# Performance work log

Hardware: AMD Instinct MI355X
Metric: run time of the kernel (lower is better)

## Reference

```python
import jax, jax.numpy as jnp
import numpy as np

IN_SZ = 256
OUT_SZ = 256
N_CHAN = 1024
RANK = 4  # min(4, IN_SZ*OUT_SZ)
B = 256
N = 2048


def setup_inputs() -> dict:
    key = jax.random.key(0)
    k_x, k_idx, k_u, k_v, k_b = jax.random.split(key, 5)
    x = jax.random.normal(k_x, (B, N, IN_SZ), dtype=jnp.float32)
    indices = jax.random.randint(k_idx, (B,), 0, N_CHAN)
    # init per reset_parameters(const=1.0)
    bound_u = np.sqrt(3.0 / RANK)              # fan_out of weights_U [C, r] is r
    weights_U = jax.random.uniform(k_u, (N_CHAN, RANK), jnp.float32, -bound_u, bound_u)
    bound_v = np.sqrt(1.0 / (IN_SZ * OUT_SZ))  # fan_out of weights_V [r, in*out]
    weights_V = jax.random.uniform(k_v, (RANK, IN_SZ * OUT_SZ), jnp.float32, -bound_v, bound_v)
    bound_b = np.sqrt(1.0 / RANK)
    bias = jax.random.uniform(k_b, (N_CHAN, 1, OUT_SZ), jnp.float32, -bound_b, bound_b)
    return {"x": x, "indices": indices, "weights_U": weights_U,
            "weights_V": weights_V, "bias": bias}


def reference(x, indices, weights_U, weights_V, bias):
    # weight synthesis: gather U rows first, then low-rank expand (same math as
    # full (U@V)[indices], without materializing unused channels)
    w = (weights_U[indices] @ weights_V).reshape(-1, IN_SZ, OUT_SZ)  # [B, in, out]
    out = jnp.einsum('bni,bio->bno', x, w)                            # [B, N, out]
    out = out + bias[indices]                                         # [B,1,out] broadcast
    return out
```

## Files before the change

kernel.cpp:

```cpp
#include <hip/hip_runtime.h>
#include <cstdint>

typedef __attribute__((ext_vector_type(8))) short short8;
typedef __attribute__((ext_vector_type(4))) float f32x4;

constexpr int SEQ   = 2048;
constexpr int INSZ  = 256;
constexpr int OUTSZ = 256;

__device__ __forceinline__ ushort f2bf(float f) {
  union { float f; uint32_t u; } v; v.f = f;
  uint32_t u = v.u;
  return (ushort)((u + 0x7FFFu + ((u >> 16) & 1u)) >> 16);
}
__device__ __forceinline__ uint32_t pk2(float a, float b) {
  return (uint32_t)f2bf(a) | ((uint32_t)f2bf(b) << 16);
}

__global__ __launch_bounds__(256) void synth_w(
    const float* __restrict__ U, const float* __restrict__ V,
    const int* __restrict__ idx, ushort* __restrict__ wsW)
{
  const int b   = blockIdx.y;
  const int kb  = blockIdx.x;
  const int tid = threadIdx.x;
  const int ch  = idx[b];
  const float u0 = U[ch*4+0], u1 = U[ch*4+1], u2 = U[ch*4+2], u3 = U[ch*4+3];

  __shared__ ushort tile[64][260];

  const int o4    = (tid & 63) * 4;
  const int kbase = (tid >> 6) * 16;
  for (int kk = 0; kk < 16; ++kk) {
    const int k  = kbase + kk;
    const int gk = kb*64 + k;
    const float* vp = V + (size_t)gk*OUTSZ + o4;
    float4 a = *(const float4*)(vp);
    float4 c = *(const float4*)(vp + 65536);
    float4 d = *(const float4*)(vp + 131072);
    float4 e = *(const float4*)(vp + 196608);
    ushort4 pkv;
    pkv.x = f2bf(u0*a.x + u1*c.x + u2*d.x + u3*e.x);
    pkv.y = f2bf(u0*a.y + u1*c.y + u2*d.y + u3*e.y);
    pkv.z = f2bf(u0*a.z + u1*c.z + u2*d.z + u3*e.z);
    pkv.w = f2bf(u0*a.w + u1*c.w + u2*d.w + u3*e.w);
    *(ushort4*)(&tile[k][o4]) = pkv;
  }
  __syncthreads();

  for (int s = 0; s < 8; ++s) {
    const int c      = s*256 + tid;
    const int kshalf = c >> 10;
    const int nb     = (c >> 6) & 15;
    const int lane   = c & 63;
    const int o      = nb*16 + (lane & 15);
    const int k0     = kshalf*32 + (lane >> 4)*8;
    uint4 pkv;
    pkv.x = (uint32_t)tile[k0+0][o] | ((uint32_t)tile[k0+1][o] << 16);
    pkv.y = (uint32_t)tile[k0+2][o] | ((uint32_t)tile[k0+3][o] << 16);
    pkv.z = (uint32_t)tile[k0+4][o] | ((uint32_t)tile[k0+5][o] << 16);
    pkv.w = (uint32_t)tile[k0+6][o] | ((uint32_t)tile[k0+7][o] << 16);
    uint4* dst = (uint4*)(wsW + (size_t)b*65536 + (size_t)(2*kb + kshalf)*8192
                              + nb*512 + lane*8);
    *dst = pkv;
  }
}

__global__ __launch_bounds__(256, 4) void lr_gemm(
    const float* __restrict__ x, const int* __restrict__ idx,
    const float* __restrict__ bias, const ushort* __restrict__ wsW,
    float* __restrict__ out)
{
  __shared__ ushort ldsA[64*256];

  const int wg  = blockIdx.x;
  const int swz = (wg & 7) * 1024 + (wg >> 3);
  const int b     = swz >> 5;
  const int n0    = (swz & 31) * 64;

  const int tid  = threadIdx.x;
  const int lane = tid & 63;
  const int wave = tid >> 6;
  const int hi16 = lane >> 4;
  const int lo16 = lane & 15;

  const float* xb = x + ((size_t)b*SEQ + n0)*INSZ;

  #pragma unroll
  for (int it = 0; it < 8; ++it) {
    const int row = it*8 + (tid >> 5);
    const int c8  = tid & 31;
    const float* src = xb + (size_t)row*INSZ + c8*8;
    float4 f0 = *(const float4*)(src);
    float4 f1 = *(const float4*)(src + 4);
    uint4 pkv;
    pkv.x = pk2(f0.x, f0.y); pkv.y = pk2(f0.z, f0.w);
    pkv.z = pk2(f1.x, f1.y); pkv.w = pk2(f1.z, f1.w);
    *(uint4*)((char*)ldsA + row*512 + ((c8*16) ^ ((row & 7) << 4))) = pkv;
  }
  __syncthreads();

  f32x4 acc[4][4] = {};
  const int sx = (lo16 & 7) << 4;
  const ushort* wbp = wsW + (size_t)b*65536 + (size_t)(wave*4)*512 + lane*8;
  const char*   aB  = (const char*)ldsA + lo16*512;

  #pragma unroll
  for (int k5 = 0; k5 < 8; ++k5) {
    short8 bf[4], af[4];
    #pragma unroll
    for (int n = 0; n < 4; ++n)
      bf[n] = *(const short8*)(wbp + k5*8192 + n*512);
    #pragma unroll
    for (int m = 0; m < 4; ++m)
      af[m] = *(const short8*)(aB + m*8192 + ((k5*64 + hi16*16) ^ sx));
    #pragma unroll
    for (int m = 0; m < 4; ++m)
      #pragma unroll
      for (int n = 0; n < 4; ++n)
        acc[m][n] = __builtin_amdgcn_mfma_f32_16x16x32_bf16(af[m], bf[n], acc[m][n], 0, 0, 0);
  }

  const int ch = idx[b];
  const float* bb = bias + (size_t)ch*OUTSZ;
  float bv[4];
  #pragma unroll
  for (int n = 0; n < 4; ++n) bv[n] = bb[wave*64 + n*16 + lo16];

  float* outb = out + ((size_t)b*SEQ + n0)*OUTSZ;
  #pragma unroll
  for (int m = 0; m < 4; ++m) {
    const int rbase = m*16 + hi16*4;
    #pragma unroll
    for (int n = 0; n < 4; ++n) {
      const int col = wave*64 + n*16 + lo16;
      #pragma unroll
      for (int j = 0; j < 4; ++j) {
        outb[(size_t)(rbase + j)*OUTSZ + col] = acc[m][n][j] + bv[n];
      }
    }
  }
}

extern "C" void kernel_launch(void* const* d_in, const int* in_sizes, int n_in,
                              void* d_out, int out_size, void* d_ws, size_t ws_size,
                              hipStream_t stream) {
  const float* x    = (const float*)d_in[0];
  const int*   idx  = (const int*)d_in[1];
  const float* U    = (const float*)d_in[2];
  const float* V    = (const float*)d_in[3];
  const float* bias = (const float*)d_in[4];
  float* out  = (float*)d_out;
  ushort* wsW = (ushort*)d_ws;

  synth_w<<<dim3(4, 256), 256, 0, stream>>>(U, V, idx, wsW);
  lr_gemm<<<8192, 256, 0, stream>>>(x, idx, bias, wsW, out);
}
```

Measured before the change: 254.3 us.

## Load x directly from global into MFMA registers, dropping LDS staging

The GEMM kernel no longer stages the bf16-converted x tile in shared memory behind a barrier. Each wave now loads its own x fragments straight from global memory, converting to bf16 in registers. The launch-bounds occupancy hint is lowered from 4 to 3 to leave room for more registers. Every x row is now fetched and converted by all four waves, about four times the global/L2 reads of x. The per-lane loads are also less coalesced, against the saved LDS traffic and sync.

```diff
diff --git a/kernel.cpp b/kernel.cpp
--- a/kernel.cpp
+++ b/kernel.cpp
@@ -3,6 +3,7 @@
 
 typedef __attribute__((ext_vector_type(8))) short short8;
 typedef __attribute__((ext_vector_type(4))) float f32x4;
+typedef __attribute__((ext_vector_type(4))) uint32_t u32x4;
 
 constexpr int SEQ   = 2048;
 constexpr int INSZ  = 256;
@@ -66,17 +67,15 @@
   }
 }
 
-__global__ __launch_bounds__(256, 4) void lr_gemm(
+__global__ __launch_bounds__(256, 3) void lr_gemm(
     const float* __restrict__ x, const int* __restrict__ idx,
     const float* __restrict__ bias, const ushort* __restrict__ wsW,
     float* __restrict__ out)
 {
-  __shared__ ushort ldsA[64*256];
-
   const int wg  = blockIdx.x;
   const int swz = (wg & 7) * 1024 + (wg >> 3);
-  const int b     = swz >> 5;
-  const int n0    = (swz & 31) * 64;
+  const int b   = swz >> 5;
+  const int n0  = (swz & 31) * 64;
 
   const int tid  = threadIdx.x;
   const int lane = tid & 63;
@@ -84,36 +83,27 @@
   const int hi16 = lane >> 4;
   const int lo16 = lane & 15;
 
-  const float* xb = x + ((size_t)b*SEQ + n0)*INSZ;
-
-  #pragma unroll
-  for (int it = 0; it < 8; ++it) {
-    const int row = it*8 + (tid >> 5);
-    const int c8  = tid & 31;
-    const float* src = xb + (size_t)row*INSZ + c8*8;
-    float4 f0 = *(const float4*)(src);
-    float4 f1 = *(const float4*)(src + 4);
-    uint4 pkv;
-    pkv.x = pk2(f0.x, f0.y); pkv.y = pk2(f0.z, f0.w);
-    pkv.z = pk2(f1.x, f1.y); pkv.w = pk2(f1.z, f1.w);
-    *(uint4*)((char*)ldsA + row*512 + ((c8*16) ^ ((row & 7) << 4))) = pkv;
-  }
-  __syncthreads();
+  const float*  xa  = x + ((size_t)b*SEQ + n0 + lo16)*INSZ + hi16*8;
+  const ushort* wbp = wsW + (size_t)b*65536 + wave*2048 + lane*8;
 
   f32x4 acc[4][4] = {};
-  const int sx = (lo16 & 7) << 4;
-  const ushort* wbp = wsW + (size_t)b*65536 + (size_t)(wave*4)*512 + lane*8;
-  const char*   aB  = (const char*)ldsA + lo16*512;
 
   #pragma unroll
   for (int k5 = 0; k5 < 8; ++k5) {
     short8 bf[4], af[4];
     #pragma unroll
     for (int n = 0; n < 4; ++n)
-      bf[n] = *(const short8*)(wbp + k5*8192 + n*512);
+      bf[n] = *(const short8*)(wbp + (size_t)k5*8192 + n*512);
     #pragma unroll
-    for (int m = 0; m < 4; ++m)
-      af[m] = *(const short8*)(aB + m*8192 + ((k5*64 + hi16*16) ^ sx));
+    for (int m = 0; m < 4; ++m) {
+      const float* ap = xa + (size_t)m*16*INSZ + k5*32;
+      float4 f0 = *(const float4*)(ap);
+      float4 f1 = *(const float4*)(ap + 4);
+      u32x4 pk;
+      pk.x = pk2(f0.x, f0.y); pk.y = pk2(f0.z, f0.w);
+      pk.z = pk2(f1.x, f1.y); pk.w = pk2(f1.z, f1.w);
+      af[m] = __builtin_bit_cast(short8, pk);
+    }
     #pragma unroll
     for (int m = 0; m < 4; ++m)
       #pragma unroll
```

Result: slower. 418.4 us (+64.5%).

## Stage GEMM epilogue through LDS for vectorized stores and prefetch B fragments

Applied to the files above, without the earlier changes.

The output epilogue now writes accumulators into a padded LDS buffer (unioned with the A tile) in two 32-row halves, then emits coalesced float4 row stores instead of scattered 4-byte stores. Separately, the B-fragment global loads are software-pipelined one k-step ahead using double registers. The LDS staging adds barriers and extra LDS traffic, and the prefetch raises register pressure under the 4-wave occupancy bound.

```diff
diff --git a/kernel.cpp b/kernel.cpp
--- a/kernel.cpp
+++ b/kernel.cpp
@@ -66,17 +66,22 @@
   }
 }
 
+union SmemT {
+  ushort a[64*256];
+  float  e[32*260];
+};
+
 __global__ __launch_bounds__(256, 4) void lr_gemm(
     const float* __restrict__ x, const int* __restrict__ idx,
     const float* __restrict__ bias, const ushort* __restrict__ wsW,
     float* __restrict__ out)
 {
-  __shared__ ushort ldsA[64*256];
+  __shared__ SmemT sm;
 
   const int wg  = blockIdx.x;
   const int swz = (wg & 7) * 1024 + (wg >> 3);
-  const int b     = swz >> 5;
-  const int n0    = (swz & 31) * 64;
+  const int b   = swz >> 5;
+  const int n0  = (swz & 31) * 64;
 
   const int tid  = threadIdx.x;
   const int lane = tid & 63;
@@ -84,7 +89,13 @@
   const int hi16 = lane >> 4;
   const int lo16 = lane & 15;
 
-  const float* xb = x + ((size_t)b*SEQ + n0)*INSZ;
+  const float*  xb  = x + ((size_t)b*SEQ + n0)*INSZ;
+  const ushort* wbp = wsW + (size_t)b*65536 + wave*2048 + lane*8;
+
+  short8 bcur[4], bnxt[4];
+  #pragma unroll
+  for (int n = 0; n < 4; ++n)
+    bcur[n] = *(const short8*)(wbp + n*512);
 
   #pragma unroll
   for (int it = 0; it < 8; ++it) {
@@ -96,21 +107,22 @@
     uint4 pkv;
     pkv.x = pk2(f0.x, f0.y); pkv.y = pk2(f0.z, f0.w);
     pkv.z = pk2(f1.x, f1.y); pkv.w = pk2(f1.z, f1.w);
-    *(uint4*)((char*)ldsA + row*512 + ((c8*16) ^ ((row & 7) << 4))) = pkv;
+    *(uint4*)((char*)sm.a + row*512 + ((c8*16) ^ ((row & 7) << 4))) = pkv;
   }
   __syncthreads();
 
   f32x4 acc[4][4] = {};
   const int sx = (lo16 & 7) << 4;
-  const ushort* wbp = wsW + (size_t)b*65536 + (size_t)(wave*4)*512 + lane*8;
-  const char*   aB  = (const char*)ldsA + lo16*512;
+  const char* aB = (const char*)sm.a + lo16*512;
 
   #pragma unroll
   for (int k5 = 0; k5 < 8; ++k5) {
-    short8 bf[4], af[4];
-    #pragma unroll
-    for (int n = 0; n < 4; ++n)
-      bf[n] = *(const short8*)(wbp + k5*8192 + n*512);
+    if (k5 < 7) {
+      #pragma unroll
+      for (int n = 0; n < 4; ++n)
+        bnxt[n] = *(const short8*)(wbp + (size_t)(k5+1)*8192 + n*512);
+    }
+    short8 af[4];
     #pragma unroll
     for (int m = 0; m < 4; ++m)
       af[m] = *(const short8*)(aB + m*8192 + ((k5*64 + hi16*16) ^ sx));
@@ -118,7 +130,9 @@
     for (int m = 0; m < 4; ++m)
       #pragma unroll
       for (int n = 0; n < 4; ++n)
-        acc[m][n] = __builtin_amdgcn_mfma_f32_16x16x32_bf16(af[m], bf[n], acc[m][n], 0, 0, 0);
+        acc[m][n] = __builtin_amdgcn_mfma_f32_16x16x32_bf16(af[m], bcur[n], acc[m][n], 0, 0, 0);
+    #pragma unroll
+    for (int n = 0; n < 4; ++n) bcur[n] = bnxt[n];
   }
 
   const int ch = idx[b];
@@ -129,15 +143,26 @@
 
   float* outb = out + ((size_t)b*SEQ + n0)*OUTSZ;
   #pragma unroll
-  for (int m = 0; m < 4; ++m) {
-    const int rbase = m*16 + hi16*4;
+  for (int p = 0; p < 2; ++p) {
+    __syncthreads();
     #pragma unroll
-    for (int n = 0; n < 4; ++n) {
-      const int col = wave*64 + n*16 + lo16;
+    for (int mm = 0; mm < 2; ++mm) {
+      const int m = p*2 + mm;
+      const int r = mm*16 + hi16*4;
       #pragma unroll
-      for (int j = 0; j < 4; ++j) {
-        outb[(size_t)(rbase + j)*OUTSZ + col] = acc[m][n][j] + bv[n];
+      for (int n = 0; n < 4; ++n) {
+        const int col = wave*64 + n*16 + lo16;
+        #pragma unroll
+        for (int j = 0; j < 4; ++j)
+          sm.e[(r + j)*260 + col] = acc[m][n][j] + bv[n];
       }
+    }
+    __syncthreads();
+    #pragma unroll
+    for (int q = 0; q < 8; ++q) {
+      const int rl = wave*8 + q;
+      float4 v = *(const float4*)&sm.e[rl*260 + lane*4];
+      *(float4*)(outb + (size_t)(p*32 + rl)*OUTSZ + lane*4) = v;
     }
   }
 }
```

Measured after the change: 248.3 us. 1.02x faster.
